# Optimization experiments

Hardware: AMD Instinct MI355X
Metric: run time of the kernel (lower is better)

## Reference

```python
import jax, jax.numpy as jnp
import numpy as np

MODEL_DIM = 1024
NUM_HEADS = 16
D_K = MODEL_DIM // NUM_HEADS  # 64
MAX_SEQ_LEN = 4096


def _xavier(key, shape):
    fan_in, fan_out = shape[1], shape[0]
    limit = np.sqrt(6.0 / (fan_in + fan_out)).astype(np.float32)
    return jax.random.uniform(key, shape, jnp.float32, -limit, limit)


def setup_inputs() -> dict:
    key = jax.random.key(0)
    ks = jax.random.split(key, 6)
    x = jax.random.normal(ks[0], (2, 2048, MODEL_DIM), jnp.float32)
    wq = _xavier(ks[1], (MODEL_DIM, MODEL_DIM))
    wk = _xavier(ks[2], (MODEL_DIM, MODEL_DIM))
    wv = _xavier(ks[3], (MODEL_DIM, MODEL_DIM))
    wo = _xavier(ks[4], (MODEL_DIM, MODEL_DIM))
    bq = jnp.zeros((MODEL_DIM,), jnp.float32)
    bk = jnp.zeros((MODEL_DIM,), jnp.float32)
    bv = jnp.zeros((MODEL_DIM,), jnp.float32)
    bo = jnp.zeros((MODEL_DIM,), jnp.float32)
    # precomputed rotary tables (cos/sin of position * theta^(-2i/d))
    half = D_K // 2
    theta = jnp.power(10000.0, jnp.arange(half, dtype=jnp.float32) * (-2.0 / D_K))
    angles = jnp.arange(MAX_SEQ_LEN, dtype=jnp.float32)[:, None] * theta[None, :]
    rot_cos = jnp.cos(angles)  # [max_seq_len, d_k//2]
    rot_sin = jnp.sin(angles)
    return {"x": x, "wq": wq, "bq": bq, "wk": wk, "bk": bk,
            "wv": wv, "bv": bv, "wo": wo, "bo": bo,
            "rot_cos": rot_cos, "rot_sin": rot_sin}


def reference(x, wq, bq, wk, bk, wv, bv, wo, bo, rot_cos, rot_sin):
    b, t, m = x.shape
    h, d = NUM_HEADS, m // NUM_HEADS
    # NOTE: original uses .view (reshape), NOT transpose, to split heads.
    q = (x @ wq.T + bq).reshape(b, h, t, d)
    k = (x @ wk.T + bk).reshape(b, h, t, d)
    v = (x @ wv.T + bv).reshape(b, h, t, d)
    # Faithful to original: rotation matrix indexed by scalar position == seq_len,
    # so every token uses the SAME rotation angle (position t).
    c = rot_cos[t]  # [d//2]
    s = rot_sin[t]

    def rope(u):
        ur = u.reshape(b, h, t, d // 2, 2)
        re, im = ur[..., 0], ur[..., 1]
        return jnp.stack([re * c - im * s, re * s + im * c], axis=-1).reshape(b, h, t, d)

    q, k = rope(q), rope(k)
    scores = jnp.einsum('bhqd,bhkd->bhqk', q, k) / np.float32(np.sqrt(d))
    p = jax.nn.softmax(scores, axis=-1)  # mask='none', dropout=0.0
    o = jnp.einsum('bhqk,bhkd->bhqd', p, v)
    o = o.transpose(0, 2, 1, 3).reshape(b, t, m)  # 'b h t d -> b t (h d)'
    return o @ wo.T + bo
```

## Files before the change

kernel.cpp:

```cpp
#include <hip/hip_runtime.h>
#include <hip/hip_bf16.h>
#include <stdint.h>


typedef __attribute__((ext_vector_type(8))) short bf16x8;
typedef bf16x8 __attribute__((may_alias)) bf16x8_a;
typedef __attribute__((ext_vector_type(4))) float f32x4;
typedef __attribute__((ext_vector_type(2))) unsigned int u32x2;
typedef u32x2 __attribute__((may_alias)) u32x2_a;

__device__ inline unsigned short f2b(float f) {
  union { float f; unsigned int u; } x; x.f = f;
  unsigned int r = x.u + 0x7fffu + ((x.u >> 16) & 1u);
  return (unsigned short)(r >> 16);
}

__device__ inline unsigned cvtpk_bf16(float lo, float hi) {
  unsigned r;
  asm("v_cvt_pk_bf16_f32 %0, %1, %2" : "=v"(r) : "v"(lo), "v"(hi));
  return r;
}

__global__ __launch_bounds__(256) void cvt_all(
    const float* __restrict__ x,
    const float* __restrict__ w0, const float* __restrict__ w1,
    const float* __restrict__ w2, const float* __restrict__ w3,
    unsigned short* __restrict__ xb,
    unsigned short* __restrict__ o0, unsigned short* __restrict__ o1,
    unsigned short* __restrict__ o2, unsigned short* __restrict__ o3) {
  int bid = blockIdx.x;
  const float* in; unsigned short* out; int i;
  if (bid < 4096) { in = x; out = xb; i = bid * 256 + threadIdx.x; }
  else {
    int w = (bid - 4096) >> 10;
    in = (w == 0) ? w0 : (w == 1) ? w1 : (w == 2) ? w2 : w3;
    out = (w == 0) ? o0 : (w == 1) ? o1 : (w == 2) ? o2 : o3;
    i = ((bid - 4096) & 1023) * 256 + threadIdx.x;
  }
  float4 v = reinterpret_cast<const float4*>(in)[i];
  ushort4 o;
  o.x = f2b(v.x); o.y = f2b(v.y); o.z = f2b(v.z); o.w = f2b(v.w);
  reinterpret_cast<ushort4*>(out)[i] = o;
}

template<int MODE>
__global__ __launch_bounds__(256) void gemm_bt(
    const unsigned short* __restrict__ A,
    const unsigned short* __restrict__ W0, const unsigned short* __restrict__ W1,
    const float* __restrict__ b0, const float* __restrict__ b1,
    unsigned short* __restrict__ o0, unsigned short* __restrict__ o1,
    float* __restrict__ of, int M, int N, int K)
{
  const int tid = threadIdx.x;
  const int lane = tid & 63;
  const int wid = tid >> 6;
  const int q4 = lane >> 4;
  const int l15 = lane & 15;
  const int wr = wid >> 1, wc = wid & 1;

  const unsigned short* W = W0; const float* bias = b0; unsigned short* ob = o0;
  if (MODE == 0 && blockIdx.z == 1) { W = W1; bias = b1; ob = o1; }

  __shared__ __align__(16) unsigned short sA[2][128 * 64];
  __shared__ __align__(16) unsigned short sB[2][128 * 64];
  char* sAc = (char*)sA;
  char* sBc = (char*)sB;

  f32x4 acc[4][4];
#pragma unroll
  for (int i = 0; i < 4; ++i)
#pragma unroll
    for (int j = 0; j < 4; ++j) acc[i][j] = (f32x4){0.f, 0.f, 0.f, 0.f};

  const size_t rowA0 = (size_t)blockIdx.x * 128;
  const size_t rowB0 = (size_t)blockIdx.y * 128;

  auto stage = [&](int bs, int k0) {
#pragma unroll
    for (int it = 0; it < 4; ++it) {
      int Loff = it * 4096 + wid * 1024;
      int L = Loff + lane * 16;
      int row = L >> 7;
      int csrc = ((L >> 4) & 7) ^ (row & 7);
      const unsigned short* ga = A + (rowA0 + row) * K + k0 + csrc * 8;
      const unsigned short* gw = W + (rowB0 + row) * K + k0 + csrc * 8;
      __builtin_amdgcn_global_load_lds((const __attribute__((address_space(1))) void*)ga,
                                       (__attribute__((address_space(3))) void*)(sAc + bs * 16384 + Loff),
                                       16, 0, 0);
      __builtin_amdgcn_global_load_lds((const __attribute__((address_space(1))) void*)gw,
                                       (__attribute__((address_space(3))) void*)(sBc + bs * 16384 + Loff),
                                       16, 0, 0);
    }
  };

  stage(0, 0);

  const int NT = K >> 6;
  for (int t = 0; t < NT; ++t) {
    const int cur = t & 1;
    __syncthreads();
    if (t + 1 < NT) stage(cur ^ 1, (t + 1) * 64);

#pragma unroll
    for (int ks = 0; ks < 2; ++ks) {
      bf16x8 af[4], bfr[4];
#pragma unroll
      for (int f = 0; f < 4; ++f) {
        int ra = wr * 64 + f * 16 + l15;
        af[f] = *(const bf16x8_a*)(sAc + cur * 16384 + ra * 128 +
                                   ((ks * 64 + q4 * 16) ^ ((ra & 7) << 4)));
        int rb = wc * 64 + f * 16 + l15;
        bfr[f] = *(const bf16x8_a*)(sBc + cur * 16384 + rb * 128 +
                                    ((ks * 64 + q4 * 16) ^ ((rb & 7) << 4)));
      }
      __builtin_amdgcn_s_setprio(1);
#pragma unroll
      for (int i = 0; i < 4; ++i)
#pragma unroll
        for (int j = 0; j < 4; ++j) {
          if (MODE == 2)
            acc[i][j] = __builtin_amdgcn_mfma_f32_16x16x32_bf16(bfr[j], af[i], acc[i][j], 0, 0, 0);
          else
            acc[i][j] = __builtin_amdgcn_mfma_f32_16x16x32_bf16(af[i], bfr[j], acc[i][j], 0, 0, 0);
        }
      __builtin_amdgcn_s_setprio(0);
    }
  }

  if (MODE == 2) {
    const int bh = (int)rowA0 >> 7;
#pragma unroll
    for (int i = 0; i < 4; ++i) {
      const int tt = wr * 64 + i * 16 + l15;
      const size_t rb = (size_t)bh * 131072 + tt;
#pragma unroll
      for (int j = 0; j < 4; ++j) {
#pragma unroll
        for (int r = 0; r < 4; ++r) {
          const int c = (int)rowB0 + wc * 64 + j * 16 + q4 * 4 + r;
          ob[rb + (size_t)(c & 63) * 2048 + (size_t)(c >> 6) * 128] = f2b(acc[i][j][r] + bias[c]);
        }
      }
    }
  } else {
#pragma unroll
    for (int i = 0; i < 4; ++i) {
      int row = (int)rowA0 + wr * 64 + i * 16 + q4 * 4;
#pragma unroll
      for (int j = 0; j < 4; ++j) {
        int col = (int)rowB0 + wc * 64 + j * 16 + l15;
        float bv = bias[col];
        if (MODE == 0 && blockIdx.z == 1) {
#pragma unroll
          for (int r = 0; r < 4; ++r) {
            size_t a = (size_t)((row + r) >> 7) * 131072 +
                       (size_t)(((col >> 6) << 7) + ((row + r) & 127)) * 64 + (col & 63);
            ob[a] = f2b(acc[i][j][r] + bv);
          }
        } else {
#pragma unroll
          for (int r = 0; r < 4; ++r) {
            float v = acc[i][j][r] + bv;
            if (MODE == 0) ob[(size_t)(row + r) * N + col] = f2b(v * 0.18033688f);
            else           of[(size_t)(row + r) * N + col] = v;
          }
        }
      }
    }
  }
}

__global__ __launch_bounds__(256, 2) void attn_kernel(
    const unsigned short* __restrict__ Qg,
    const unsigned short* __restrict__ Kg,
    const unsigned short* __restrict__ VTg,
    unsigned short* __restrict__ ctx)
{
  const int tid = threadIdx.x;
  const int lane = tid & 63;
  const int wid = tid >> 6;
  const int q4 = lane >> 4;
  const int l15 = lane & 15;

  const int bid = blockIdx.x;
  const int bh = (bid & 7) * 4 + ((bid >> 3) >> 4);
  const int qt = (bid >> 3) & 15;
  const int b = bh >> 4, h = bh & 15;
  const size_t base = (size_t)bh * 131072;
  const unsigned short* Qh = Qg + base;
  const unsigned short* Kh = Kg + base;
  const unsigned short* VTh = VTg + base;
  const int q0 = qt * 128;

  __shared__ __align__(16) unsigned short sK[2][64 * 64];
  __shared__ __align__(16) unsigned short sV[2][64 * 64];
  __shared__ __align__(16) unsigned short sP[4][32 * 64];

  bf16x8 qf[2][2];
#pragma unroll
  for (int s = 0; s < 2; ++s)
#pragma unroll
    for (int ks = 0; ks < 2; ++ks)
      qf[s][ks] = *(const bf16x8*)(Qh + (size_t)(q0 + wid * 32 + s * 16 + l15) * 64 + ks * 32 + q4 * 8);

  const int rr = tid >> 3;
  const int colB = ((tid & 7) ^ (rr & 7)) * 8;
  const unsigned short* gK = Kh + (size_t)rr * 64 + colB;
  const unsigned short* gV = VTh + (size_t)rr * 2048 + colB;
  char* sKc = (char*)sK;
  char* sVc = (char*)sV;
  char* sPw = (char*)sP + wid * 4096;

  auto stage = [&](int bs, int kv0) {
    __builtin_amdgcn_global_load_lds(
        (const __attribute__((address_space(1))) void*)(gK + (size_t)kv0 * 64),
        (__attribute__((address_space(3))) void*)(sKc + bs * 8192 + wid * 1024), 16, 0, 0);
    __builtin_amdgcn_global_load_lds(
        (const __attribute__((address_space(1))) void*)(gK + (size_t)kv0 * 64 + 2048),
        (__attribute__((address_space(3))) void*)(sKc + bs * 8192 + 4096 + wid * 1024), 16, 0, 0);
    __builtin_amdgcn_global_load_lds(
        (const __attribute__((address_space(1))) void*)(gV + kv0),
        (__attribute__((address_space(3))) void*)(sVc + bs * 8192 + wid * 1024), 16, 0, 0);
    __builtin_amdgcn_global_load_lds(
        (const __attribute__((address_space(1))) void*)(gV + kv0 + 65536),
        (__attribute__((address_space(3))) void*)(sVc + bs * 8192 + 4096 + wid * 1024), 16, 0, 0);
  };

  f32x4 oacc[2][4];
#pragma unroll
  for (int s = 0; s < 2; ++s)
#pragma unroll
    for (int fn = 0; fn < 4; ++fn) oacc[s][fn] = (f32x4){0.f, 0.f, 0.f, 0.f};
  float m_run[2] = {-INFINITY, -INFINITY};
  float l_run[2] = {0.f, 0.f};

  stage(0, 0);

  for (int t = 0; t < 32; ++t) {
    const int cur = t & 1;
    __syncthreads();
    if (t < 31) stage(cur ^ 1, (t + 1) * 64);

    f32x4 sc[2][4];
#pragma unroll
    for (int s = 0; s < 2; ++s)
#pragma unroll
      for (int fm = 0; fm < 4; ++fm) sc[s][fm] = (f32x4){0.f, 0.f, 0.f, 0.f};
    __builtin_amdgcn_s_setprio(1);
#pragma unroll
    for (int ks = 0; ks < 2; ++ks) {
#pragma unroll
      for (int fm = 0; fm < 4; ++fm) {
        const int rk = fm * 16 + l15;
        bf16x8_a kf = *(const bf16x8_a*)(sKc + cur * 8192 + rk * 128 +
                                         ((ks * 64 + q4 * 16) ^ ((rk & 7) << 4)));
        sc[0][fm] = __builtin_amdgcn_mfma_f32_16x16x32_bf16(kf, qf[0][ks], sc[0][fm], 0, 0, 0);
        sc[1][fm] = __builtin_amdgcn_mfma_f32_16x16x32_bf16(kf, qf[1][ks], sc[1][fm], 0, 0, 0);
      }
    }
    __builtin_amdgcn_s_setprio(0);

#pragma unroll
    for (int s = 0; s < 2; ++s) {
      float mx = fmaxf(fmaxf(fmaxf(sc[s][0][0], sc[s][0][1]), fmaxf(sc[s][0][2], sc[s][0][3])),
                       fmaxf(fmaxf(sc[s][1][0], sc[s][1][1]), fmaxf(sc[s][1][2], sc[s][1][3])));
      mx = fmaxf(mx, fmaxf(fmaxf(fmaxf(sc[s][2][0], sc[s][2][1]), fmaxf(sc[s][2][2], sc[s][2][3])),
                           fmaxf(fmaxf(sc[s][3][0], sc[s][3][1]), fmaxf(sc[s][3][2], sc[s][3][3]))));
      mx = fmaxf(mx, __shfl_xor(mx, 16));
      mx = fmaxf(mx, __shfl_xor(mx, 32));
      if (!__all(mx <= m_run[s] + 11.54f)) {
        const float mnew = fmaxf(m_run[s], mx);
        const float sc_o = __builtin_amdgcn_exp2f(m_run[s] - mnew);
        l_run[s] *= sc_o;
        m_run[s] = mnew;
#pragma unroll
        for (int r = 0; r < 4; ++r) {
          const float so = __shfl(sc_o, (lane & 48) | (q4 * 4 + r));
#pragma unroll
          for (int fn = 0; fn < 4; ++fn) oacc[s][fn][r] *= so;
        }
      }
      float rs = 0.f;
#pragma unroll
      for (int fm = 0; fm < 4; ++fm)
#pragma unroll
        for (int r = 0; r < 4; ++r) {
          sc[s][fm][r] = __builtin_amdgcn_exp2f(sc[s][fm][r] - m_run[s]);
          rs += sc[s][fm][r];
        }
      rs += __shfl_xor(rs, 16);
      rs += __shfl_xor(rs, 32);
      l_run[s] += rs;

      char* rowp = sPw + (s * 16 + l15) * 128;
#pragma unroll
      for (int fm = 0; fm < 4; ++fm) {
        u32x2 pk;
        pk[0] = cvtpk_bf16(sc[s][fm][0], sc[s][fm][1]);
        pk[1] = cvtpk_bf16(sc[s][fm][2], sc[s][fm][3]);
        *(u32x2_a*)(rowp + ((fm * 32 + q4 * 8) ^ ((l15 & 7) << 4))) = pk;
      }
    }
    asm volatile("s_waitcnt lgkmcnt(0)" ::: "memory");
    __builtin_amdgcn_sched_barrier(0);

#pragma unroll
    for (int ks2 = 0; ks2 < 2; ++ks2) {
      bf16x8 pf[2];
#pragma unroll
      for (int s = 0; s < 2; ++s)
        pf[s] = *(const bf16x8_a*)(sPw + (s * 16 + l15) * 128 +
                                   ((ks2 * 64 + q4 * 16) ^ ((l15 & 7) << 4)));
      __builtin_amdgcn_s_setprio(1);
#pragma unroll
      for (int fn = 0; fn < 4; ++fn) {
        const int rv = fn * 16 + l15;
        bf16x8_a vf = *(const bf16x8_a*)(sVc + cur * 8192 + rv * 128 +
                                         ((ks2 * 64 + q4 * 16) ^ ((rv & 7) << 4)));
        oacc[0][fn] = __builtin_amdgcn_mfma_f32_16x16x32_bf16(pf[0], vf, oacc[0][fn], 0, 0, 0);
        oacc[1][fn] = __builtin_amdgcn_mfma_f32_16x16x32_bf16(pf[1], vf, oacc[1][fn], 0, 0, 0);
      }
      __builtin_amdgcn_s_setprio(0);
    }
  }

#pragma unroll
  for (int s = 0; s < 2; ++s) {
    const float inv = 1.0f / l_run[s];
#pragma unroll
    for (int r = 0; r < 4; ++r) {
      const float ir = __shfl(inv, (lane & 48) | (q4 * 4 + r));
      const int trow = q0 + wid * 32 + s * 16 + q4 * 4 + r;
      const size_t ro = ((size_t)b * 2048 + trow) * 1024 + h * 64;
#pragma unroll
      for (int fn = 0; fn < 4; ++fn)
        ctx[ro + fn * 16 + l15] = f2b(oacc[s][fn][r] * ir);
    }
  }
}

extern "C" void kernel_launch(void* const* d_in, const int* in_sizes, int n_in,
                              void* d_out, int out_size, void* d_ws, size_t ws_size,
                              hipStream_t stream) {
  const float* x  = (const float*)d_in[0];
  const float* wq = (const float*)d_in[1];
  const float* bq = (const float*)d_in[2];
  const float* wk = (const float*)d_in[3];
  const float* bk = (const float*)d_in[4];
  const float* wv = (const float*)d_in[5];
  const float* bv = (const float*)d_in[6];
  const float* wo = (const float*)d_in[7];
  const float* bo = (const float*)d_in[8];

  char* ws = (char*)d_ws;
  unsigned short* xb  = (unsigned short*)(ws);
  unsigned short* wqb = (unsigned short*)(ws + 8388608);
  unsigned short* wkb = (unsigned short*)(ws + 10485760);
  unsigned short* wvb = (unsigned short*)(ws + 12582912);
  unsigned short* wob = (unsigned short*)(ws + 14680064);
  unsigned short* Qb  = (unsigned short*)(ws + 16777216);
  unsigned short* Kb  = (unsigned short*)(ws + 25165824);
  unsigned short* VTb = (unsigned short*)(ws + 33554432);
  unsigned short* ctx = xb;

  cvt_all<<<8192, 256, 0, stream>>>(x, wq, wk, wv, wo, xb, wqb, wkb, wvb, wob);

  gemm_bt<0><<<dim3(32, 8, 2), 256, 0, stream>>>(
      xb, wqb, wkb, bq, bk, Qb, Kb, nullptr, 4096, 1024, 1024);
  gemm_bt<2><<<dim3(32, 8, 1), 256, 0, stream>>>(
      xb, wvb, nullptr, bv, nullptr, VTb, nullptr, nullptr, 4096, 1024, 1024);

  attn_kernel<<<dim3(512), dim3(256), 0, stream>>>(Qb, Kb, VTb, ctx);

  gemm_bt<1><<<dim3(32, 8, 1), 256, 0, stream>>>(
      ctx, wob, nullptr, bo, nullptr, nullptr, nullptr,
      (float*)d_out, 4096, 1024, 1024);
}
```

Before: 136.9 us.

## Load attention K/V fragments directly from global into registers per wave

```diff
diff --git a/kernel.cpp b/kernel.cpp
--- a/kernel.cpp
+++ b/kernel.cpp
@@ -170,61 +170,39 @@
   }
 }
 
-__global__ __launch_bounds__(256, 2) void attn_kernel(
+__global__ __launch_bounds__(64, 2) void attn_kernel(
     const unsigned short* __restrict__ Qg,
     const unsigned short* __restrict__ Kg,
     const unsigned short* __restrict__ VTg,
     unsigned short* __restrict__ ctx)
 {
-  const int tid = threadIdx.x;
-  const int lane = tid & 63;
-  const int wid = tid >> 6;
+  const int lane = threadIdx.x;
   const int q4 = lane >> 4;
   const int l15 = lane & 15;
 
   const int bid = blockIdx.x;
-  const int bh = (bid & 7) * 4 + ((bid >> 3) >> 4);
-  const int qt = (bid >> 3) & 15;
+  const int r = bid >> 3;
+  const int bh = (bid & 7) * 4 + (r >> 6);
+  const int qw = r & 63;
   const int b = bh >> 4, h = bh & 15;
   const size_t base = (size_t)bh * 131072;
   const unsigned short* Qh = Qg + base;
   const unsigned short* Kh = Kg + base;
   const unsigned short* VTh = VTg + base;
-  const int q0 = qt * 128;
-
-  __shared__ __align__(16) unsigned short sK[2][64 * 64];
-  __shared__ __align__(16) unsigned short sV[2][64 * 64];
-  __shared__ __align__(16) unsigned short sP[4][32 * 64];
+  const int q0 = qw * 32;
+
+  __shared__ __align__(16) unsigned short sP[32 * 64];
 
   bf16x8 qf[2][2];
 #pragma unroll
   for (int s = 0; s < 2; ++s)
 #pragma unroll
     for (int ks = 0; ks < 2; ++ks)
-      qf[s][ks] = *(const bf16x8*)(Qh + (size_t)(q0 + wid * 32 + s * 16 + l15) * 64 + ks * 32 + q4 * 8);
-
-  const int rr = tid >> 3;
-  const int colB = ((tid & 7) ^ (rr & 7)) * 8;
-  const unsigned short* gK = Kh + (size_t)rr * 64 + colB;
-  const unsigned short* gV = VTh + (size_t)rr * 2048 + colB;
-  char* sKc = (char*)sK;
-  char* sVc = (char*)sV;
-  char* sPw = (char*)sP + wid * 4096;
-
-  auto stage = [&](int bs, int kv0) {
-    __builtin_amdgcn_global_load_lds(
-        (const __attribute__((address_space(1))) void*)(gK + (size_t)kv0 * 64),
-        (__attribute__((address_space(3))) void*)(sKc + bs * 8192 + wid * 1024), 16, 0, 0);
-    __builtin_amdgcn_global_load_lds(
-        (const __attribute__((address_space(1))) void*)(gK + (size_t)kv0 * 64 + 2048),
-        (__attribute__((address_space(3))) void*)(sKc + bs * 8192 + 4096 + wid * 1024), 16, 0, 0);
-    __builtin_amdgcn_global_load_lds(
-        (const __attribute__((address_space(1))) void*)(gV + kv0),
-        (__attribute__((address_space(3))) void*)(sVc + bs * 8192 + wid * 1024), 16, 0, 0);
-    __builtin_amdgcn_global_load_lds(
-        (const __attribute__((address_space(1))) void*)(gV + kv0 + 65536),
-        (__attribute__((address_space(3))) void*)(sVc + bs * 8192 + 4096 + wid * 1024), 16, 0, 0);
-  };
+      qf[s][ks] = *(const bf16x8*)(Qh + (size_t)(q0 + s * 16 + l15) * 64 + ks * 32 + q4 * 8);
+
+  const unsigned short* kbase = Kh + (size_t)(l15 * 64 + q4 * 8);
+  const unsigned short* vbase = VTh + (size_t)(l15 * 2048 + q4 * 8);
+  char* sPc = (char*)sP;
 
   f32x4 oacc[2][4];
 #pragma unroll
@@ -234,12 +212,20 @@
   float m_run[2] = {-INFINITY, -INFINITY};
   float l_run[2] = {0.f, 0.f};
 
-  stage(0, 0);
-
   for (int t = 0; t < 32; ++t) {
-    const int cur = t & 1;
-    __syncthreads();
-    if (t < 31) stage(cur ^ 1, (t + 1) * 64);
+    const int kv0 = t * 64;
+
+    bf16x8 kf[2][4], vf[2][4];
+#pragma unroll
+    for (int ks = 0; ks < 2; ++ks)
+#pragma unroll
+      for (int fm = 0; fm < 4; ++fm)
+        kf[ks][fm] = *(const bf16x8_a*)(kbase + (size_t)kv0 * 64 + fm * 1024 + ks * 32);
+#pragma unroll
+    for (int ks2 = 0; ks2 < 2; ++ks2)
+#pragma unroll
+      for (int fn = 0; fn < 4; ++fn)
+        vf[ks2][fn] = *(const bf16x8_a*)(vbase + (size_t)fn * 32768 + kv0 + ks2 * 32);
 
     f32x4 sc[2][4];
 #pragma unroll
@@ -248,16 +234,12 @@
       for (int fm = 0; fm < 4; ++fm) sc[s][fm] = (f32x4){0.f, 0.f, 0.f, 0.f};
     __builtin_amdgcn_s_setprio(1);
 #pragma unroll
-    for (int ks = 0; ks < 2; ++ks) {
+    for (int ks = 0; ks < 2; ++ks)
 #pragma unroll
       for (int fm = 0; fm < 4; ++fm) {
-        const int rk = fm * 16 + l15;
-        bf16x8_a kf = *(const bf16x8_a*)(sKc + cur * 8192 + rk * 128 +
-                                         ((ks * 64 + q4 * 16) ^ ((rk & 7) << 4)));
-        sc[0][fm] = __builtin_amdgcn_mfma_f32_16x16x32_bf16(kf, qf[0][ks], sc[0][fm], 0, 0, 0);
-        sc[1][fm] = __builtin_amdgcn_mfma_f32_16x16x32_bf16(kf, qf[1][ks], sc[1][fm], 0, 0, 0);
-      }
-    }
+        sc[0][fm] = __builtin_amdgcn_mfma_f32_16x16x32_bf16(kf[ks][fm], qf[0][ks], sc[0][fm], 0, 0, 0);
+        sc[1][fm] = __builtin_amdgcn_mfma_f32_16x16x32_bf16(kf[ks][fm], qf[1][ks], sc[1][fm], 0, 0, 0);
+      }
     __builtin_amdgcn_s_setprio(0);
 
 #pragma unroll
@@ -274,25 +256,25 @@
         l_run[s] *= sc_o;
         m_run[s] = mnew;
 #pragma unroll
-        for (int r = 0; r < 4; ++r) {
-          const float so = __shfl(sc_o, (lane & 48) | (q4 * 4 + r));
-#pragma unroll
-          for (int fn = 0; fn < 4; ++fn) oacc[s][fn][r] *= so;
+        for (int rr = 0; rr < 4; ++rr) {
+          const float so = __shfl(sc_o, (lane & 48) | (q4 * 4 + rr));
+#pragma unroll
+          for (int fn = 0; fn < 4; ++fn) oacc[s][fn][rr] *= so;
         }
       }
       float rs = 0.f;
 #pragma unroll
       for (int fm = 0; fm < 4; ++fm)
 #pragma unroll
-        for (int r = 0; r < 4; ++r) {
-          sc[s][fm][r] = __builtin_amdgcn_exp2f(sc[s][fm][r] - m_run[s]);
-          rs += sc[s][fm][r];
+        for (int rr = 0; rr < 4; ++rr) {
+          sc[s][fm][rr] = __builtin_amdgcn_exp2f(sc[s][fm][rr] - m_run[s]);
+          rs += sc[s][fm][rr];
         }
       rs += __shfl_xor(rs, 16);
       rs += __shfl_xor(rs, 32);
       l_run[s] += rs;
 
-      char* rowp = sPw + (s * 16 + l15) * 128;
+      char* rowp = sPc + (s * 16 + l15) * 128;
 #pragma unroll
       for (int fm = 0; fm < 4; ++fm) {
         u32x2 pk;
@@ -309,16 +291,13 @@
       bf16x8 pf[2];
 #pragma unroll
       for (int s = 0; s < 2; ++s)
-        pf[s] = *(const bf16x8_a*)(sPw + (s * 16 + l15) * 128 +
+        pf[s] = *(const bf16x8_a*)(sPc + (s * 16 + l15) * 128 +
                                    ((ks2 * 64 + q4 * 16) ^ ((l15 & 7) << 4)));
       __builtin_amdgcn_s_setprio(1);
 #pragma unroll
       for (int fn = 0; fn < 4; ++fn) {
-        const int rv = fn * 16 + l15;
-        bf16x8_a vf = *(const bf16x8_a*)(sVc + cur * 8192 + rv * 128 +
-                                         ((ks2 * 64 + q4 * 16) ^ ((rv & 7) << 4)));
-        oacc[0][fn] = __builtin_amdgcn_mfma_f32_16x16x32_bf16(pf[0], vf, oacc[0][fn], 0, 0, 0);
-        oacc[1][fn] = __builtin_amdgcn_mfma_f32_16x16x32_bf16(pf[1], vf, oacc[1][fn], 0, 0, 0);
+        oacc[0][fn] = __builtin_amdgcn_mfma_f32_16x16x32_bf16(pf[0], vf[ks2][fn], oacc[0][fn], 0, 0, 0);
+        oacc[1][fn] = __builtin_amdgcn_mfma_f32_16x16x32_bf16(pf[1], vf[ks2][fn], oacc[1][fn], 0, 0, 0);
       }
       __builtin_amdgcn_s_setprio(0);
     }
@@ -328,13 +307,13 @@
   for (int s = 0; s < 2; ++s) {
     const float inv = 1.0f / l_run[s];
 #pragma unroll
-    for (int r = 0; r < 4; ++r) {
-      const float ir = __shfl(inv, (lane & 48) | (q4 * 4 + r));
-      const int trow = q0 + wid * 32 + s * 16 + q4 * 4 + r;
+    for (int rr = 0; rr < 4; ++rr) {
+      const float ir = __shfl(inv, (lane & 48) | (q4 * 4 + rr));
+      const int trow = q0 + s * 16 + q4 * 4 + rr;
       const size_t ro = ((size_t)b * 2048 + trow) * 1024 + h * 64;
 #pragma unroll
       for (int fn = 0; fn < 4; ++fn)
-        ctx[ro + fn * 16 + l15] = f2b(oacc[s][fn][r] * ir);
+        ctx[ro + fn * 16 + l15] = f2b(oacc[s][fn][rr] * ir);
     }
   }
 }
@@ -370,7 +349,7 @@
   gemm_bt<2><<<dim3(32, 8, 1), 256, 0, stream>>>(
       xb, wvb, nullptr, bv, nullptr, VTb, nullptr, nullptr, 4096, 1024, 1024);
 
-  attn_kernel<<<dim3(512), dim3(256), 0, stream>>>(Qb, Kb, VTb, ctx);
+  attn_kernel<<<dim3(2048), dim3(64), 0, stream>>>(Qb, Kb, VTb, ctx);
 
   gemm_bt<1><<<dim3(32, 8, 1), 256, 0, stream>>>(
       ctx, wob, nullptr, bo, nullptr, nullptr, nullptr,
```

Result: slower. 194.4 us (+42.0%).
